# Optimization experiments

Measured on AMD Instinct MI355X. Metric: run time of the kernel, lower is better.

Reference implementation:

```python
import jax, jax.numpy as jnp
import numpy as np

D_MODEL = 1024
N_HEADS = 16
SCALES = (1, 2, 4, 8)
B, S = 4, 2048
NS = len(SCALES)
E = D_MODEL // NS        # per-scale embed dim = 256
H = N_HEADS // NS        # per-scale heads = 4
DK = E // H              # head dim = 64


def setup_inputs() -> dict:
    key = jax.random.key(0)
    ks = jax.random.split(key, 6)
    sc = lambda fan_in: 1.0 / np.sqrt(fan_in)
    return {
        "x": jax.random.normal(ks[0], (B, S, D_MODEL), jnp.float32),
        # per-scale projection Linear(d_model -> E), stacked over scales
        "proj_W": jax.random.normal(ks[1], (NS, D_MODEL, E), jnp.float32) * sc(D_MODEL),
        "proj_b": jnp.zeros((NS, E), jnp.float32),
        # per-scale MultiheadAttention in_proj (q,k,v packed) and out_proj
        "in_W": jax.random.normal(ks[2], (NS, E, 3 * E), jnp.float32) * sc(E),
        "in_b": jnp.zeros((NS, 3 * E), jnp.float32),
        "out_W": jax.random.normal(ks[3], (NS, E, E), jnp.float32) * sc(E),
        "out_b": jnp.zeros((NS, E), jnp.float32),
        # fusion: Linear(d_model -> d_model) + LayerNorm (dropout is identity in eval)
        "fus_W": jax.random.normal(ks[4], (D_MODEL, D_MODEL), jnp.float32) * sc(D_MODEL),
        "fus_b": jnp.zeros((D_MODEL,), jnp.float32),
        "ln_g": jnp.ones((D_MODEL,), jnp.float32),
        "ln_b": jnp.zeros((D_MODEL,), jnp.float32),
    }


def _mha(x, in_W, in_b, out_W, out_b):
    # torch nn.MultiheadAttention, batch_first, eval mode, need_weights=True
    b, L, _ = x.shape
    qkv = x @ in_W + in_b                       # [b, L, 3E]
    q, k, v = jnp.split(qkv, 3, axis=-1)
    heads = lambda t: t.reshape(b, L, H, DK).transpose(0, 2, 1, 3)  # [b,h,L,dk]
    q, k, v = heads(q), heads(k), heads(v)
    scores = jnp.einsum('bhqd,bhkd->bhqk', q, k) / np.sqrt(DK).astype(np.float32)
    probs = jax.nn.softmax(scores, axis=-1)
    o = jnp.einsum('bhqk,bhkd->bhqd', probs, v).transpose(0, 2, 1, 3).reshape(b, L, E)
    return o @ out_W + out_b, probs.mean(axis=1)  # averaged over heads: [b,L,L]


def _upsample(y, s):
    # Faithful vectorization of the torch interpolation loop when S % s == 0:
    # full[k*s + j] = (1 - j/s)*y[k] + (j/s)*y[k+1], with zero right-neighbor
    # for the last block (torch reads attn_out_full[S-1] while it is still 0).
    if s == 1:
        return y
    b, K, d = y.shape
    y_next = jnp.concatenate([y[:, 1:], jnp.zeros_like(y[:, :1])], axis=1)
    alpha = (jnp.arange(s, dtype=y.dtype) / s)[None, None, :, None]  # [1,1,s,1]
    full = (1.0 - alpha) * y[:, :, None, :] + alpha * y_next[:, :, None, :]
    return full.reshape(b, K * s, d)


def reference(x, proj_W, proj_b, in_W, in_b, out_W, out_b, fus_W, fus_b, ln_g, ln_b):
    scale_outputs = []
    w0 = None
    for i, s in enumerate(SCALES):
        x_scale = x @ proj_W[i] + proj_b[i]        # [B,S,E]
        x_sub = x_scale[:, ::s, :]                 # strided subsequence [B,S//s,E]
        y, w = _mha(x_sub, in_W[i], in_b[i], out_W[i], out_b[i])
        scale_outputs.append(_upsample(y, s))
        if i == 0:
            w0 = w                                  # combined_weights = first scale's weights
    z = jnp.concatenate(scale_outputs, axis=-1) @ fus_W + fus_b
    mu = z.mean(-1, keepdims=True)
    var = z.var(-1, keepdims=True)
    fused = (z - mu) / jnp.sqrt(var + 1e-5) * ln_g + ln_b
    return fused, w0
```

## Files before the change

### kernel.cpp

```cpp
#include <hip/hip_runtime.h>
#include <hip/hip_bf16.h>


typedef short bh8 __attribute__((ext_vector_type(8)));
typedef float f32x4 __attribute__((ext_vector_type(4)));

__device__ __forceinline__ ushort f2b(float f) {
    __hip_bfloat16 h = __float2bfloat16(f);
    return *reinterpret_cast<ushort*>(&h);
}
__device__ __forceinline__ float b2f(ushort u) {
    __hip_bfloat16 h;
    *reinterpret_cast<ushort*>(&h) = u;
    return __bfloat162float(h);
}

__global__ __launch_bounds__(256) void cvt_kernel(
    const float* __restrict__ s, ushort* __restrict__ d, long n)
{
    long i = ((long)blockIdx.x * 256 + threadIdx.x) * 4;
    if (i >= n) return;
    float4 v = *(const float4*)(s + i);
    ushort4 o;
    o.x = f2b(v.x); o.y = f2b(v.y); o.z = f2b(v.z); o.w = f2b(v.w);
    *(ushort4*)(d + i) = o;
}

__global__ __launch_bounds__(256) void wtrans_kernel(
    const float* __restrict__ src, ushort* __restrict__ dst, int K, int N)
{
    __shared__ float Ls[32][33];
    const int n0 = blockIdx.x * 32, k0 = blockIdx.y * 32;
    const float* s = src + (long)blockIdx.z * K * N;
    ushort* d = dst + (long)blockIdx.z * N * K;
    const int tid = threadIdx.x;
    #pragma unroll
    for (int it = 0; it < 4; ++it) {
        int f = tid + it * 256;
        int kc = f >> 5, rn = f & 31;
        Ls[kc][rn] = s[(long)(k0 + kc) * N + n0 + rn];
    }
    __syncthreads();
    #pragma unroll
    for (int it = 0; it < 2; ++it) {
        int f = tid + it * 256;
        int rn = f >> 4, kc2 = (f & 15) * 2;
        ushort2 o;
        o.x = f2b(Ls[kc2][rn]);
        o.y = f2b(Ls[kc2 + 1][rn]);
        *(ushort2*)&d[(long)(n0 + rn) * K + k0 + kc2] = o;
    }
}

template<int MODE>
__global__ __launch_bounds__(256) void gemm_ms(
    const ushort* __restrict__ A, const ushort* __restrict__ Wt,
    const float* __restrict__ bias, ushort* __restrict__ C)
{
    constexpr int K = (MODE == 0) ? 1024 : 256;
    constexpr int N = (MODE == 1) ? 768 : 256;
    __shared__ ushort As[128][72];
    __shared__ ushort Bs[128][72];

    const int tid = threadIdx.x;
    const int wave = tid >> 6, lane = tid & 63;
    const int lm = lane & 15, quad = lane >> 4;
    const int wm = (wave & 1) * 64, wn = (wave >> 1) * 64;
    const int m0 = blockIdx.x * 128, n0 = blockIdx.y * 128;
    const int s = (m0 >= 14336) ? 3 : ((m0 >= 12288) ? 2 : ((m0 >= 8192) ? 1 : 0));
    const ushort* Wp = Wt + (long)s * N * K;
    const float* bp_ = bias + s * N;

    f32x4 acc[4][4];
    #pragma unroll
    for (int i = 0; i < 4; ++i)
        #pragma unroll
        for (int j = 0; j < 4; ++j) {
            f32x4 zz = {0.f, 0.f, 0.f, 0.f};
            acc[i][j] = zz;
        }

    const int r0 = tid >> 3, k8 = (tid & 7) * 8;
    const ushort* ap[4];
    #pragma unroll
    for (int it = 0; it < 4; ++it) {
        int m = m0 + r0 + it * 32;
        if (MODE == 0) {
            int t = m - (16384 - (16384 >> s));
            int b = t >> (11 - s);
            int tt = t - (b << (11 - s));
            ap[it] = A + ((long)(b * 2048) + ((long)tt << s)) * 1024 + k8;
        } else {
            ap[it] = A + (long)m * K + k8;
        }
    }
    const ushort* bp[4];
    #pragma unroll
    for (int it = 0; it < 4; ++it)
        bp[it] = Wp + (long)(n0 + r0 + it * 32) * K + k8;

    for (int k0 = 0; k0 < K; k0 += 64) {
        #pragma unroll
        for (int it = 0; it < 4; ++it)
            *(bh8*)&As[r0 + it * 32][k8] = *(const bh8*)(ap[it] + k0);
        #pragma unroll
        for (int it = 0; it < 4; ++it)
            *(bh8*)&Bs[r0 + it * 32][k8] = *(const bh8*)(bp[it] + k0);
        __syncthreads();
        #pragma unroll
        for (int ks = 0; ks < 2; ++ks) {
            bh8 af[4], bfv[4];
            #pragma unroll
            for (int i = 0; i < 4; ++i)
                af[i] = *(const bh8*)&As[wm + i * 16 + lm][ks * 32 + quad * 8];
            #pragma unroll
            for (int j = 0; j < 4; ++j)
                bfv[j] = *(const bh8*)&Bs[wn + j * 16 + lm][ks * 32 + quad * 8];
            #pragma unroll
            for (int i = 0; i < 4; ++i)
                #pragma unroll
                for (int j = 0; j < 4; ++j)
                    acc[i][j] = __builtin_amdgcn_mfma_f32_16x16x32_bf16(
                        af[i], bfv[j], acc[i][j], 0, 0, 0);
        }
        __syncthreads();
    }

    float bv[4]; int cols[4];
    #pragma unroll
    for (int j = 0; j < 4; ++j) {
        cols[j] = n0 + wn + j * 16 + lm;
        bv[j] = bp_[cols[j]];
    }
    #pragma unroll
    for (int i = 0; i < 4; ++i) {
        int mb = m0 + wm + i * 16 + quad * 4;
        #pragma unroll
        for (int j = 0; j < 4; ++j)
            #pragma unroll
            for (int r = 0; r < 4; ++r)
                C[(long)(mb + r) * N + cols[j]] = f2b(acc[i][j][r] + bv[j]);
    }
}

__global__ __launch_bounds__(256) void vtrans_ms(
    const ushort* __restrict__ qkvb, ushort* __restrict__ vTb)
{
    __shared__ ushort Ls[64][72];
    const int bid = blockIdx.x;
    const int s = (bid >= 896) ? 3 : ((bid >= 768) ? 2 : ((bid >= 512) ? 1 : 0));
    const int rel = bid - ((s == 0) ? 0 : ((s == 1) ? 512 : ((s == 2) ? 768 : 896)));
    const int L = 2048 >> s;
    const int z = rel >> (5 - s);
    const int kt = rel & ((32 >> s) - 1);
    const int b = z >> 2, h = z & 3;
    const ushort* src = qkvb + (long)(16384 - (16384 >> s)) * 768
                        + (long)b * L * 768 + 512 + h * 64;
    const int k0 = kt * 64;
    const int tid = threadIdx.x;
    const int kk = tid >> 3, d8 = (tid & 7) * 8;
    #pragma unroll
    for (int it = 0; it < 2; ++it) {
        int k = kk + it * 32;
        bh8 v = *(const bh8*)(src + (long)(k0 + k) * 768 + d8);
        ushort tmp[8];
        *(bh8*)tmp = v;
        #pragma unroll
        for (int j = 0; j < 8; ++j) Ls[d8 + j][k] = tmp[j];
    }
    __syncthreads();
    ushort* dst = vTb + (long)(4096 - (4096 >> s)) * 1024 + (long)z * 64 * L;
    #pragma unroll
    for (int it = 0; it < 2; ++it) {
        int d = kk + it * 32;
        *(bh8*)(dst + (long)d * L + k0 + d8) = *(const bh8*)&Ls[d][d8];
    }
}

__global__ __launch_bounds__(256, 3) void attn_ms(
    const ushort* __restrict__ qkvb, const ushort* __restrict__ vTb,
    ushort* __restrict__ ob, float* __restrict__ msc, float* __restrict__ invl)
{
    __shared__ ushort Ks[128 * 72];
    __shared__ ushort Vs[64 * 136];
    __shared__ ushort Ps[64 * 136];

    const int bid = blockIdx.x;
    const int s = (bid >= 896) ? 3 : ((bid >= 768) ? 2 : ((bid >= 512) ? 1 : 0));
    const int rel = bid - ((s == 0) ? 0 : ((s == 1) ? 512 : ((s == 2) ? 768 : 896)));
    const int L = 2048 >> s;
    const int z = rel >> (5 - s);
    const int qt = rel & ((32 >> s) - 1);
    const int b = z >> 2, h = z & 3;
    const int Rr16 = 16384 - (16384 >> s);
    const ushort* qbase = qkvb + (long)Rr16 * 768 + (long)b * L * 768 + h * 64;
    const ushort* kbase = qbase + 256;
    const ushort* vbase = vTb + (long)(4096 - (4096 >> s)) * 1024 + (long)z * 64 * L;
    ushort* o = ob + (long)Rr16 * 256;

    const int tid = threadIdx.x;
    const int wave = tid >> 6, lane = tid & 63;
    const int lm = lane & 15, quad = lane >> 4;
    const int wm = wave * 16;
    const int q0 = qt * 64;
    const int r0 = tid >> 3, k8 = (tid & 7) * 8;
    const int vd0 = tid >> 4, vc8 = (tid & 15) * 8;

    #pragma unroll
    for (int it = 0; it < 2; ++it) {
        int row = r0 + it * 32;
        *(bh8*)&Ps[row * 136 + k8] = *(const bh8*)(qbase + (long)(q0 + row) * 768 + k8);
    }
    __syncthreads();
    bh8 qf[2];
    #pragma unroll
    for (int ks = 0; ks < 2; ++ks)
        qf[ks] = *(const bh8*)&Ps[(wm + lm) * 136 + ks * 32 + quad * 8];

    f32x4 oc[4];
    #pragma unroll
    for (int nj = 0; nj < 4; ++nj) {
        f32x4 zz = {0.f, 0.f, 0.f, 0.f};
        oc[nj] = zz;
    }
    float m_run[4], l_run[4];
    #pragma unroll
    for (int rr = 0; rr < 4; ++rr) { m_run[rr] = -3.0e38f; l_run[rr] = 0.f; }

    for (int k0 = 0; k0 < L; k0 += 128) {
        #pragma unroll
        for (int it = 0; it < 4; ++it) {
            int row = r0 + it * 32;
            *(bh8*)&Ks[row * 72 + k8] = *(const bh8*)(kbase + (long)(k0 + row) * 768 + k8);
        }
        #pragma unroll
        for (int it = 0; it < 4; ++it) {
            int d = vd0 + it * 16;
            *(bh8*)&Vs[d * 136 + vc8] = *(const bh8*)(vbase + (long)d * L + k0 + vc8);
        }
        __syncthreads();

        f32x4 sc[8];
        #pragma unroll
        for (int nj = 0; nj < 8; ++nj) {
            f32x4 zz = {0.f, 0.f, 0.f, 0.f};
            sc[nj] = zz;
        }
        #pragma unroll
        for (int ks = 0; ks < 2; ++ks)
            #pragma unroll
            for (int nj = 0; nj < 8; ++nj) {
                bh8 kf = *(const bh8*)&Ks[(nj * 16 + lm) * 72 + ks * 32 + quad * 8];
                sc[nj] = __builtin_amdgcn_mfma_f32_16x16x32_bf16(qf[ks], kf, sc[nj], 0, 0, 0);
            }

        #pragma unroll
        for (int rr = 0; rr < 4; ++rr) {
            float t = sc[0][rr];
            #pragma unroll
            for (int nj = 1; nj < 8; ++nj) t = fmaxf(t, sc[nj][rr]);
            t = fmaxf(t, __shfl_xor(t, 1));
            t = fmaxf(t, __shfl_xor(t, 2));
            t = fmaxf(t, __shfl_xor(t, 4));
            t = fmaxf(t, __shfl_xor(t, 8));
            float mo = m_run[rr];
            float mn = fmaxf(mo, t);
            float alpha = __expf(0.125f * (mo - mn));
            m_run[rr] = mn;
            float rs = 0.f;
            int prow = (wm + quad * 4 + rr) * 136;
            #pragma unroll
            for (int nj = 0; nj < 8; ++nj) {
                float p = __expf(0.125f * (sc[nj][rr] - mn));
                rs += p;
                Ps[prow + nj * 16 + lm] = f2b(p);
            }
            rs += __shfl_xor(rs, 1);
            rs += __shfl_xor(rs, 2);
            rs += __shfl_xor(rs, 4);
            rs += __shfl_xor(rs, 8);
            l_run[rr] = l_run[rr] * alpha + rs;
            #pragma unroll
            for (int nj = 0; nj < 4; ++nj) oc[nj][rr] *= alpha;
        }

        #pragma unroll
        for (int kst = 0; kst < 4; ++kst) {
            bh8 pf = *(const bh8*)&Ps[(wm + lm) * 136 + kst * 32 + quad * 8];
            #pragma unroll
            for (int nj = 0; nj < 4; ++nj) {
                bh8 vf = *(const bh8*)&Vs[(nj * 16 + lm) * 136 + kst * 32 + quad * 8];
                oc[nj] = __builtin_amdgcn_mfma_f32_16x16x32_bf16(pf, vf, oc[nj], 0, 0, 0);
            }
        }
        __syncthreads();
    }

    #pragma unroll
    for (int rr = 0; rr < 4; ++rr) {
        float il = 1.f / l_run[rr];
        int q = q0 + wm + quad * 4 + rr;
        if (s == 0 && lm == 0) {
            msc[z * 2048 + q] = 0.125f * m_run[rr];
            invl[z * 2048 + q] = il;
        }
        long rbase = ((long)(b * L + q)) * 256 + h * 64;
        #pragma unroll
        for (int nj = 0; nj < 4; ++nj)
            o[rbase + nj * 16 + lm] = f2b(oc[nj][rr] * il);
    }
}

__global__ __launch_bounds__(256, 2) void w0_recompute(
    const ushort* __restrict__ qkv,
    const float* __restrict__ msc, const float* __restrict__ invl,
    float* __restrict__ w0)
{
    const int L = 2048;
    __shared__ ushort Qs[128 * 72];
    __shared__ ushort Ks[128 * 72];
    __shared__ ushort Ws[128 * 136];

    const int tid = threadIdx.x;
    const int wave = tid >> 6, lane = tid & 63;
    const int lm = lane & 15, quad = lane >> 4;
    const int wm = wave * 32;
    const int q0 = blockIdx.x * 128, k0 = blockIdx.y * 128;
    const int b = blockIdx.z;
    const int r0 = tid >> 3, k8 = (tid & 7) * 8;

    f32x4 acc[2][8];
    #pragma unroll
    for (int mi = 0; mi < 2; ++mi)
        #pragma unroll
        for (int nj = 0; nj < 8; ++nj) {
            f32x4 zz = {0.f, 0.f, 0.f, 0.f};
            acc[mi][nj] = zz;
        }

    for (int h = 0; h < 4; ++h) {
        const ushort* qb = qkv + (long)b * L * 768 + h * 64;
        const ushort* kb = qb + 256;
        #pragma unroll
        for (int it = 0; it < 4; ++it) {
            int r = r0 + it * 32;
            *(bh8*)&Qs[r * 72 + k8] = *(const bh8*)(qb + (long)(q0 + r) * 768 + k8);
            *(bh8*)&Ks[r * 72 + k8] = *(const bh8*)(kb + (long)(k0 + r) * 768 + k8);
        }
        __syncthreads();
        bh8 qf[2][2];
        #pragma unroll
        for (int mi = 0; mi < 2; ++mi)
            #pragma unroll
            for (int ks = 0; ks < 2; ++ks)
                qf[mi][ks] = *(const bh8*)&Qs[(wm + mi * 16 + lm) * 72 + ks * 32 + quad * 8];
        f32x4 sc[2][8];
        #pragma unroll
        for (int mi = 0; mi < 2; ++mi)
            #pragma unroll
            for (int nj = 0; nj < 8; ++nj) {
                f32x4 zz = {0.f, 0.f, 0.f, 0.f};
                sc[mi][nj] = zz;
            }
        #pragma unroll
        for (int ks = 0; ks < 2; ++ks)
            #pragma unroll
            for (int nj = 0; nj < 8; ++nj) {
                bh8 kf = *(const bh8*)&Ks[(nj * 16 + lm) * 72 + ks * 32 + quad * 8];
                #pragma unroll
                for (int mi = 0; mi < 2; ++mi)
                    sc[mi][nj] = __builtin_amdgcn_mfma_f32_16x16x32_bf16(
                        qf[mi][ks], kf, sc[mi][nj], 0, 0, 0);
            }
        const float* mz = msc + (long)(b * 4 + h) * L;
        const float* iz = invl + (long)(b * 4 + h) * L;
        #pragma unroll
        for (int mi = 0; mi < 2; ++mi)
            #pragma unroll
            for (int rr = 0; rr < 4; ++rr) {
                int q = q0 + wm + mi * 16 + quad * 4 + rr;
                float mv = mz[q], iv = iz[q];
                #pragma unroll
                for (int nj = 0; nj < 8; ++nj)
                    acc[mi][nj][rr] += __expf(0.125f * sc[mi][nj][rr] - mv) * iv;
            }
        __syncthreads();
    }

    #pragma unroll
    for (int mi = 0; mi < 2; ++mi)
        #pragma unroll
        for (int rr = 0; rr < 4; ++rr) {
            int prow = (wm + mi * 16 + quad * 4 + rr) * 136;
            #pragma unroll
            for (int nj = 0; nj < 8; ++nj)
                Ws[prow + nj * 16 + lm] = f2b(0.25f * acc[mi][nj][rr]);
        }
    __syncthreads();
    #pragma unroll
    for (int it = 0; it < 8; ++it) {
        int idx = tid + it * 256;
        int row = idx >> 4, c8 = (idx & 15) * 8;
        ushort tmp[8];
        *(bh8*)tmp = *(const bh8*)&Ws[row * 136 + c8];
        long base = ((long)b * 2048 + q0 + row) * 2048 + k0 + c8;
        float4 f0, f1;
        f0.x = b2f(tmp[0]); f0.y = b2f(tmp[1]); f0.z = b2f(tmp[2]); f0.w = b2f(tmp[3]);
        f1.x = b2f(tmp[4]); f1.y = b2f(tmp[5]); f1.z = b2f(tmp[6]); f1.w = b2f(tmp[7]);
        *(float4*)&w0[base] = f0;
        *(float4*)&w0[base + 4] = f1;
    }
}

__global__ __launch_bounds__(256) void upsample_ms(
    const ushort* __restrict__ yallb, ushort* __restrict__ ccat)
{
    const int bid = blockIdx.x;
    const int s = bid >> 11;
    const int idx = (bid & 2047) * 256 + threadIdx.x;
    const int c4 = (idx & 63) * 4;
    const int t = (idx >> 6) & 2047;
    const int b = idx >> 17;
    const int L = 2048 >> s;
    const int k = t >> s, j = t & ((1 << s) - 1);
    const float a = (float)j / (float)(1 << s);
    const ushort* y = yallb + (long)(16384 - (16384 >> s)) * 256;
    const ushort* y0p = y + ((long)(b * L + k)) * 256 + c4;
    ushort4 y0 = *(const ushort4*)y0p;
    ushort4 y1 = {0, 0, 0, 0};
    if (k + 1 < L) y1 = *(const ushort4*)(y0p + 256);
    ushort4 o;
    o.x = f2b((1.f - a) * b2f(y0.x) + a * b2f(y1.x));
    o.y = f2b((1.f - a) * b2f(y0.y) + a * b2f(y1.y));
    o.z = f2b((1.f - a) * b2f(y0.z) + a * b2f(y1.z));
    o.w = f2b((1.f - a) * b2f(y0.w) + a * b2f(y1.w));
    *(ushort4*)&ccat[((long)(b * 2048 + t)) * 1024 + s * 256 + c4] = o;
}

__global__ __launch_bounds__(256) void gemm_fus(
    const ushort* __restrict__ A, const ushort* __restrict__ Wt,
    const float* __restrict__ bias, float* __restrict__ C)
{
    const int K = 1024, N = 1024;
    __shared__ ushort As[128][72];
    __shared__ ushort Bs[128][72];
    const int tid = threadIdx.x;
    const int wave = tid >> 6, lane = tid & 63;
    const int lm = lane & 15, quad = lane >> 4;
    const int wm = (wave & 1) * 64, wn = (wave >> 1) * 64;
    const int m0 = blockIdx.x * 128, n0 = blockIdx.y * 128;

    f32x4 acc[4][4];
    #pragma unroll
    for (int i = 0; i < 4; ++i)
        #pragma unroll
        for (int j = 0; j < 4; ++j) {
            f32x4 zz = {0.f, 0.f, 0.f, 0.f};
            acc[i][j] = zz;
        }
    const int r0 = tid >> 3, k8 = (tid & 7) * 8;
    for (int k0 = 0; k0 < K; k0 += 64) {
        #pragma unroll
        for (int it = 0; it < 4; ++it) {
            int r = r0 + it * 32;
            *(bh8*)&As[r][k8] = *(const bh8*)(A + (long)(m0 + r) * K + k0 + k8);
            *(bh8*)&Bs[r][k8] = *(const bh8*)(Wt + (long)(n0 + r) * K + k0 + k8);
        }
        __syncthreads();
        #pragma unroll
        for (int ks = 0; ks < 2; ++ks) {
            bh8 af[4], bfv[4];
            #pragma unroll
            for (int i = 0; i < 4; ++i)
                af[i] = *(const bh8*)&As[wm + i * 16 + lm][ks * 32 + quad * 8];
            #pragma unroll
            for (int j = 0; j < 4; ++j)
                bfv[j] = *(const bh8*)&Bs[wn + j * 16 + lm][ks * 32 + quad * 8];
            #pragma unroll
            for (int i = 0; i < 4; ++i)
                #pragma unroll
                for (int j = 0; j < 4; ++j)
                    acc[i][j] = __builtin_amdgcn_mfma_f32_16x16x32_bf16(
                        af[i], bfv[j], acc[i][j], 0, 0, 0);
        }
        __syncthreads();
    }
    float bv[4]; int cols[4];
    #pragma unroll
    for (int j = 0; j < 4; ++j) {
        cols[j] = n0 + wn + j * 16 + lm;
        bv[j] = bias[cols[j]];
    }
    #pragma unroll
    for (int i = 0; i < 4; ++i) {
        int mb = m0 + wm + i * 16 + quad * 4;
        #pragma unroll
        for (int j = 0; j < 4; ++j)
            #pragma unroll
            for (int r = 0; r < 4; ++r)
                C[(long)(mb + r) * N + cols[j]] = acc[i][j][r] + bv[j];
    }
}

__global__ __launch_bounds__(256) void ln_kernel(
    float* __restrict__ zbuf, const float* __restrict__ g, const float* __restrict__ bta)
{
    long row = blockIdx.x;
    float* p = zbuf + row * 1024;
    const int tid = threadIdx.x;
    float v[4];
    float s = 0.f;
    #pragma unroll
    for (int j = 0; j < 4; ++j) { v[j] = p[tid + (j << 8)]; s += v[j]; }
    #pragma unroll
    for (int off = 32; off; off >>= 1) s += __shfl_xor(s, off);
    __shared__ float r0[4], r1[4];
    int wid = tid >> 6;
    if ((tid & 63) == 0) r0[wid] = s;
    __syncthreads();
    s = r0[0] + r0[1] + r0[2] + r0[3];
    float mu = s * (1.f / 1024.f);
    float q = 0.f;
    #pragma unroll
    for (int j = 0; j < 4; ++j) { float d = v[j] - mu; q += d * d; }
    #pragma unroll
    for (int off = 32; off; off >>= 1) q += __shfl_xor(q, off);
    if ((tid & 63) == 0) r1[wid] = q;
    __syncthreads();
    q = r1[0] + r1[1] + r1[2] + r1[3];
    float rstd = rsqrtf(q * (1.f / 1024.f) + 1e-5f);
    #pragma unroll
    for (int j = 0; j < 4; ++j) {
        int c = tid + (j << 8);
        p[c] = (v[j] - mu) * rstd * g[c] + bta[c];
    }
}

extern "C" void kernel_launch(void* const* d_in, const int* in_sizes, int n_in,
                              void* d_out, int out_size, void* d_ws, size_t ws_size,
                              hipStream_t stream)
{
    const float* x     = (const float*)d_in[0];
    const float* projW = (const float*)d_in[1];
    const float* projB = (const float*)d_in[2];
    const float* inW   = (const float*)d_in[3];
    const float* inB   = (const float*)d_in[4];
    const float* outW  = (const float*)d_in[5];
    const float* outB  = (const float*)d_in[6];
    const float* fusW  = (const float*)d_in[7];
    const float* fusB  = (const float*)d_in[8];
    const float* lnG   = (const float*)d_in[9];
    const float* lnB   = (const float*)d_in[10];

    float* fused  = (float*)d_out;
    float* out_w0 = fused + 8388608;

    char* w = (char*)d_ws;
    ushort* xb     = (ushort*)w; w += 16777216;
    ushort* pT     = (ushort*)w; w += 2097152;
    ushort* iT     = (ushort*)w; w += 1572864;
    ushort* oT     = (ushort*)w; w += 524288;
    ushort* fT     = (ushort*)w; w += 2097152;
    ushort* xprojb = (ushort*)w; w += 7864320;
    ushort* qkvb   = (ushort*)w; w += 23592960;
    ushort* ob     = (ushort*)w; w += 7864320;
    ushort* yallb  = (ushort*)w; w += 7864320;
    ushort* ccatb  = (ushort*)w; w += 16777216;
    ushort* vTb    = (ushort*)w; w += 7864320;
    float*  msc    = (float*)w;  w += 131072;
    float*  invl   = (float*)w;  w += 131072;

    cvt_kernel<<<8192, 256, 0, stream>>>(x, xb, 8388608);
    wtrans_kernel<<<dim3(8, 32, 4), 256, 0, stream>>>(projW, pT, 1024, 256);
    wtrans_kernel<<<dim3(24, 8, 4), 256, 0, stream>>>(inW, iT, 256, 768);
    wtrans_kernel<<<dim3(8, 8, 4), 256, 0, stream>>>(outW, oT, 256, 256);
    wtrans_kernel<<<dim3(32, 32, 1), 256, 0, stream>>>(fusW, fT, 1024, 1024);

    gemm_ms<0><<<dim3(120, 2), 256, 0, stream>>>(xb, pT, projB, xprojb);
    gemm_ms<1><<<dim3(120, 6), 256, 0, stream>>>(xprojb, iT, inB, qkvb);
    vtrans_ms<<<960, 256, 0, stream>>>(qkvb, vTb);
    attn_ms<<<960, 256, 0, stream>>>(qkvb, vTb, ob, msc, invl);
    w0_recompute<<<dim3(16, 16, 4), 256, 0, stream>>>(qkvb, msc, invl, out_w0);
    gemm_ms<2><<<dim3(120, 2), 256, 0, stream>>>(ob, oT, outB, yallb);
    upsample_ms<<<8192, 256, 0, stream>>>(yallb, ccatb);
    gemm_fus<<<dim3(64, 8), 256, 0, stream>>>(ccatb, fT, fusB, fused);
    ln_kernel<<<8192, 256, 0, stream>>>(fused, lnG, lnB);
}
```

Baseline: 347.4 us.

## Cut attention LDS, use exp2 and DPP reductions, vectorize LayerNorm

The attention kernel now shares one LDS buffer between K tiles and P tiles, adding a barrier after QK^T, and raises the launch bound to 4 blocks per CU for higher occupancy. Softmax works in base-2 with a pre-scaled running max, a raw v_exp_f32, and DPP row reductions in place of shuffles. The w0 recompute kernel aliases its W staging buffer onto Q/K storage and uses the same exp2 form. LayerNorm switches to float4 loads and stores. The extra barrier per tile and tighter register limits could offset the occupancy gain.

```diff
diff --git a/kernel.cpp b/kernel.cpp
--- a/kernel.cpp
+++ b/kernel.cpp
@@ -4,6 +4,8 @@
 
 typedef short bh8 __attribute__((ext_vector_type(8)));
 typedef float f32x4 __attribute__((ext_vector_type(4)));
+
+#define CLOG2E 0.18033688011112042f
 
 __device__ __forceinline__ ushort f2b(float f) {
     __hip_bfloat16 h = __float2bfloat16(f);
@@ -13,6 +15,31 @@
     __hip_bfloat16 h;
     *reinterpret_cast<ushort*>(&h) = u;
     return __bfloat162float(h);
+}
+__device__ __forceinline__ float fexp2(float x) {
+    float r;
+    asm("v_exp_f32 %0, %1" : "=v"(r) : "v"(x));
+    return r;
+}
+template<int CTRL>
+__device__ __forceinline__ float dpp_mv(float x) {
+    int i = __float_as_int(x);
+    int r = __builtin_amdgcn_update_dpp(i, i, CTRL, 0xF, 0xF, false);
+    return __int_as_float(r);
+}
+__device__ __forceinline__ float row_max16(float t) {
+    t = fmaxf(t, dpp_mv<0x128>(t));
+    t = fmaxf(t, dpp_mv<0x124>(t));
+    t = fmaxf(t, dpp_mv<0x122>(t));
+    t = fmaxf(t, dpp_mv<0x121>(t));
+    return t;
+}
+__device__ __forceinline__ float row_sum16(float t) {
+    t += dpp_mv<0x128>(t);
+    t += dpp_mv<0x124>(t);
+    t += dpp_mv<0x122>(t);
+    t += dpp_mv<0x121>(t);
+    return t;
 }
 
 __global__ __launch_bounds__(256) void cvt_kernel(
@@ -177,13 +204,12 @@
     }
 }
 
-__global__ __launch_bounds__(256, 3) void attn_ms(
+__global__ __launch_bounds__(256, 4) void attn_ms(
     const ushort* __restrict__ qkvb, const ushort* __restrict__ vTb,
     ushort* __restrict__ ob, float* __restrict__ msc, float* __restrict__ invl)
 {
-    __shared__ ushort Ks[128 * 72];
+    __shared__ ushort KPs[128 * 72];
     __shared__ ushort Vs[64 * 136];
-    __shared__ ushort Ps[64 * 136];
 
     const int bid = blockIdx.x;
     const int s = (bid >= 896) ? 3 : ((bid >= 768) ? 2 : ((bid >= 512) ? 1 : 0));
@@ -209,13 +235,14 @@
     #pragma unroll
     for (int it = 0; it < 2; ++it) {
         int row = r0 + it * 32;
-        *(bh8*)&Ps[row * 136 + k8] = *(const bh8*)(qbase + (long)(q0 + row) * 768 + k8);
+        *(bh8*)&KPs[row * 72 + k8] = *(const bh8*)(qbase + (long)(q0 + row) * 768 + k8);
     }
     __syncthreads();
     bh8 qf[2];
     #pragma unroll
     for (int ks = 0; ks < 2; ++ks)
-        qf[ks] = *(const bh8*)&Ps[(wm + lm) * 136 + ks * 32 + quad * 8];
+        qf[ks] = *(const bh8*)&KPs[(wm + lm) * 72 + ks * 32 + quad * 8];
+    __syncthreads();
 
     f32x4 oc[4];
     #pragma unroll
@@ -223,15 +250,15 @@
         f32x4 zz = {0.f, 0.f, 0.f, 0.f};
         oc[nj] = zz;
     }
-    float m_run[4], l_run[4];
-    #pragma unroll
-    for (int rr = 0; rr < 4; ++rr) { m_run[rr] = -3.0e38f; l_run[rr] = 0.f; }
+    float mh[4], l_run[4];
+    #pragma unroll
+    for (int rr = 0; rr < 4; ++rr) { mh[rr] = -3.0e38f; l_run[rr] = 0.f; }
 
     for (int k0 = 0; k0 < L; k0 += 128) {
         #pragma unroll
         for (int it = 0; it < 4; ++it) {
             int row = r0 + it * 32;
-            *(bh8*)&Ks[row * 72 + k8] = *(const bh8*)(kbase + (long)(k0 + row) * 768 + k8);
+            *(bh8*)&KPs[row * 72 + k8] = *(const bh8*)(kbase + (long)(k0 + row) * 768 + k8);
         }
         #pragma unroll
         for (int it = 0; it < 4; ++it) {
@@ -250,35 +277,32 @@
         for (int ks = 0; ks < 2; ++ks)
             #pragma unroll
             for (int nj = 0; nj < 8; ++nj) {
-                bh8 kf = *(const bh8*)&Ks[(nj * 16 + lm) * 72 + ks * 32 + quad * 8];
+                bh8 kf = *(const bh8*)&KPs[(nj * 16 + lm) * 72 + ks * 32 + quad * 8];
                 sc[nj] = __builtin_amdgcn_mfma_f32_16x16x32_bf16(qf[ks], kf, sc[nj], 0, 0, 0);
             }
+        __syncthreads();
 
         #pragma unroll
         for (int rr = 0; rr < 4; ++rr) {
-            float t = sc[0][rr];
-            #pragma unroll
-            for (int nj = 1; nj < 8; ++nj) t = fmaxf(t, sc[nj][rr]);
-            t = fmaxf(t, __shfl_xor(t, 1));
-            t = fmaxf(t, __shfl_xor(t, 2));
-            t = fmaxf(t, __shfl_xor(t, 4));
-            t = fmaxf(t, __shfl_xor(t, 8));
-            float mo = m_run[rr];
-            float mn = fmaxf(mo, t);
-            float alpha = __expf(0.125f * (mo - mn));
-            m_run[rr] = mn;
-            float rs = 0.f;
+            float t01 = fmaxf(sc[0][rr], sc[1][rr]);
+            float t23 = fmaxf(sc[2][rr], sc[3][rr]);
+            float t45 = fmaxf(sc[4][rr], sc[5][rr]);
+            float t67 = fmaxf(sc[6][rr], sc[7][rr]);
+            float t = fmaxf(fmaxf(t01, t23), fmaxf(t45, t67));
+            t = row_max16(t);
+            float mo = mh[rr];
+            float mn = fmaxf(mo, t * CLOG2E);
+            float alpha = fexp2(mo - mn);
+            mh[rr] = mn;
             int prow = (wm + quad * 4 + rr) * 136;
+            float p[8];
             #pragma unroll
             for (int nj = 0; nj < 8; ++nj) {
-                float p = __expf(0.125f * (sc[nj][rr] - mn));
-                rs += p;
-                Ps[prow + nj * 16 + lm] = f2b(p);
+                p[nj] = fexp2(fmaf(sc[nj][rr], CLOG2E, -mn));
+                KPs[prow + nj * 16 + lm] = f2b(p[nj]);
             }
-            rs += __shfl_xor(rs, 1);
-            rs += __shfl_xor(rs, 2);
-            rs += __shfl_xor(rs, 4);
-            rs += __shfl_xor(rs, 8);
+            float rs = ((p[0] + p[1]) + (p[2] + p[3])) + ((p[4] + p[5]) + (p[6] + p[7]));
+            rs = row_sum16(rs);
             l_run[rr] = l_run[rr] * alpha + rs;
             #pragma unroll
             for (int nj = 0; nj < 4; ++nj) oc[nj][rr] *= alpha;
@@ -286,7 +310,7 @@
 
         #pragma unroll
         for (int kst = 0; kst < 4; ++kst) {
-            bh8 pf = *(const bh8*)&Ps[(wm + lm) * 136 + kst * 32 + quad * 8];
+            bh8 pf = *(const bh8*)&KPs[(wm + lm) * 136 + kst * 32 + quad * 8];
             #pragma unroll
             for (int nj = 0; nj < 4; ++nj) {
                 bh8 vf = *(const bh8*)&Vs[(nj * 16 + lm) * 136 + kst * 32 + quad * 8];
@@ -301,7 +325,7 @@
         float il = 1.f / l_run[rr];
         int q = q0 + wm + quad * 4 + rr;
         if (s == 0 && lm == 0) {
-            msc[z * 2048 + q] = 0.125f * m_run[rr];
+            msc[z * 2048 + q] = mh[rr];
             invl[z * 2048 + q] = il;
         }
         long rbase = ((long)(b * L + q)) * 256 + h * 64;
@@ -317,9 +341,10 @@
     float* __restrict__ w0)
 {
     const int L = 2048;
-    __shared__ ushort Qs[128 * 72];
-    __shared__ ushort Ks[128 * 72];
-    __shared__ ushort Ws[128 * 136];
+    __shared__ ushort SH[18432];
+    ushort* Qs = SH;
+    ushort* Ks = SH + 9216;
+    ushort* Ws = SH;
 
     const int tid = threadIdx.x;
     const int wave = tid >> 6, lane = tid & 63;
@@ -382,7 +407,7 @@
                 float mv = mz[q], iv = iz[q];
                 #pragma unroll
                 for (int nj = 0; nj < 8; ++nj)
-                    acc[mi][nj][rr] += __expf(0.125f * sc[mi][nj][rr] - mv) * iv;
+                    acc[mi][nj][rr] += fexp2(fmaf(sc[mi][nj][rr], CLOG2E, -mv)) * iv;
             }
         __syncthreads();
     }
@@ -508,10 +533,8 @@
     long row = blockIdx.x;
     float* p = zbuf + row * 1024;
     const int tid = threadIdx.x;
-    float v[4];
-    float s = 0.f;
-    #pragma unroll
-    for (int j = 0; j < 4; ++j) { v[j] = p[tid + (j << 8)]; s += v[j]; }
+    float4 v = *(const float4*)(p + tid * 4);
+    float s = (v.x + v.y) + (v.z + v.w);
     #pragma unroll
     for (int off = 32; off; off >>= 1) s += __shfl_xor(s, off);
     __shared__ float r0[4], r1[4];
@@ -520,20 +543,22 @@
     __syncthreads();
     s = r0[0] + r0[1] + r0[2] + r0[3];
     float mu = s * (1.f / 1024.f);
-    float q = 0.f;
-    #pragma unroll
-    for (int j = 0; j < 4; ++j) { float d = v[j] - mu; q += d * d; }
+    float dx = v.x - mu, dy = v.y - mu, dz = v.z - mu, dw = v.w - mu;
+    float q = (dx * dx + dy * dy) + (dz * dz + dw * dw);
     #pragma unroll
     for (int off = 32; off; off >>= 1) q += __shfl_xor(q, off);
     if ((tid & 63) == 0) r1[wid] = q;
     __syncthreads();
     q = r1[0] + r1[1] + r1[2] + r1[3];
     float rstd = rsqrtf(q * (1.f / 1024.f) + 1e-5f);
-    #pragma unroll
-    for (int j = 0; j < 4; ++j) {
-        int c = tid + (j << 8);
-        p[c] = (v[j] - mu) * rstd * g[c] + bta[c];
-    }
+    float4 gg = *(const float4*)(g + tid * 4);
+    float4 bb = *(const float4*)(bta + tid * 4);
+    float4 o;
+    o.x = dx * rstd * gg.x + bb.x;
+    o.y = dy * rstd * gg.y + bb.y;
+    o.z = dz * rstd * gg.z + bb.z;
+    o.w = dw * rstd * gg.w + bb.w;
+    *(float4*)(p + tid * 4) = o;
 }
 
 extern "C" void kernel_launch(void* const* d_in, const int* in_sizes, int n_in,
```

Measured after the change: 358.5 us. 1.03x slower.
